# Performance work log

Hardware: AMD Instinct MI355X
Metric: run time of the kernel (lower is better)

## Reference

```python
import jax, jax.numpy as jnp
import numpy as np

MAX_STEPS = 20  # matches init kwarg max_steps


def gru_cell(x, h, W_ih, W_hh, b_ih, b_hh):
    # PyTorch GRUCell: gates ordered (reset, update, new)
    H = h.shape[1]
    gx = x @ W_ih.T + b_ih          # [B, 3H]
    gh = h @ W_hh.T + b_hh          # [B, 3H]
    r = jax.nn.sigmoid(gx[:, :H] + gh[:, :H])
    z = jax.nn.sigmoid(gx[:, H:2 * H] + gh[:, H:2 * H])
    n = jnp.tanh(gx[:, 2 * H:] + r * gh[:, 2 * H:])
    return (1.0 - z) * n + z * h


def setup_inputs() -> dict:
    key = jax.random.key(0)
    ks = jax.random.split(key, 10)
    B, E, H = 2048, 512, 1024
    bound = 1.0 / np.sqrt(H)  # torch default init scale
    uni = lambda k, shape: jax.random.uniform(k, shape, jnp.float32, -bound, bound)
    return {
        "x": jax.random.normal(ks[0], (B, E), jnp.float32),
        "W_ih": uni(ks[1], (3 * H, E)),
        "W_hh": uni(ks[2], (3 * H, H)),
        "b_ih": uni(ks[3], (3 * H,)),
        "b_hh": uni(ks[4], (3 * H,)),
        "w_out": uni(ks[5], (H,)),
        "b_out": uni(ks[6], (1,)),
        "w_lam": uni(ks[7], (H,)),
        "b_lam": uni(ks[8], (1,)),
        "u": jax.random.uniform(ks[9], (MAX_STEPS, B), jnp.float32),  # bernoulli draws
    }


def reference(x, W_ih, W_hh, b_ih, b_hh, w_out, b_out, w_lam, b_lam, u):
    B = x.shape[0]
    dt = x.dtype
    H = W_hh.shape[1]
    h0 = gru_cell(x, jnp.zeros((B, H), dt), W_ih, W_hh, b_ih, b_hh)
    steps = jnp.arange(1, MAX_STEPS + 1)

    def step(carry, inp):
        h, un_halted, halted, p_m, y_m = carry
        n_idx, u_n = inp
        lam_sig = jax.nn.sigmoid(h @ w_lam + b_lam[0])           # [B]
        lam = jnp.where(n_idx == MAX_STEPS, jnp.ones_like(lam_sig), lam_sig)
        y_n = h @ w_out + b_out[0]                                # [B]
        p_n = un_halted * lam
        un_halted = un_halted * (1.0 - lam)
        halt = (u_n < lam).astype(dt) * (1.0 - halted)            # bernoulli(lam)
        p_m = p_m * (1.0 - halt) + p_n * halt
        y_m = y_m * (1.0 - halt) + y_n * halt
        halted = halted + halt
        h = gru_cell(x, h, W_ih, W_hh, b_ih, b_hh)
        return (h, un_halted, halted, p_m, y_m), (p_n, y_n)

    init = (h0,
            jnp.ones((B,), dt),
            jnp.zeros((B,), dt),
            jnp.zeros((B,), dt),
            jnp.zeros((B,), dt))
    (_, _, _, p_m, y_m), (p, y) = jax.lax.scan(step, init, (steps, u))
    return p, y, p_m, y_m
```

## Files before the change

kernel.cpp:

```cpp
#include <hip/hip_runtime.h>
#include <math.h>


#define B_N 2048
#define E_N 512
#define H_N 1024
#define G3  3072
#define NSTEPS 20
#define BK 32
#define NT_H (H_N / BK)
#define NT_E (E_N / BK)
#define NCB  (H_N / 64)

typedef __attribute__((ext_vector_type(8))) _Float16 f16x8;
typedef __attribute__((ext_vector_type(4))) _Float16 f16x4v;
typedef __attribute__((ext_vector_type(4))) float    f32x4;

#define GLDS(src, dst) \
  __builtin_amdgcn_global_load_lds( \
      (const __attribute__((address_space(1))) void*)(src), \
      (__attribute__((address_space(3))) void*)(dst), 16, 0, 0)

__device__ __forceinline__ float sigmoidf_(float x) { return 1.0f / (1.0f + expf(-x)); }

__global__ __launch_bounds__(512, 2)
void gemm_step_mfma(const _Float16* __restrict__ h_hi_in,
                    const _Float16* __restrict__ h_lo_in,
                    const _Float16* __restrict__ Whi,
                    const _Float16* __restrict__ Wlo,
                    const float* __restrict__ b_hh,
                    const float* __restrict__ gx,
                    const float* __restrict__ w_lam,
                    const float* __restrict__ w_out,
                    _Float16* __restrict__ h_hi_out,
                    _Float16* __restrict__ h_lo_out,
                    float* __restrict__ part_lam,
                    float* __restrict__ part_out)
{
  __shared__ _Float16 lds[3][20480];
  __shared__ float pl_red[128][4], po_red[128][4];

  const int tid  = threadIdx.x;
  const int lane = tid & 63;
  const int wv   = tid >> 6;
  const int wr   = wv >> 2;
  const int wc   = wv & 3;
  const int row0 = blockIdx.y * 128;
  const int col0 = blockIdx.x * 64;
  const int cb   = blockIdx.x;

  const _Float16* srcp[5];
  int ldsoff[5];
  #pragma unroll
  for (int j = 0; j < 5; ++j) {
    const int c     = wv * 5 + j;
    const int row16 = lane >> 2;
    const int seg16 = lane & 3;
    const int seg   = (seg16 ^ (row16 & 3)) * 8;
    const _Float16* s;
    if (c < 8) {
      s = h_hi_in + (size_t)(row0 + c * 16 + row16) * H_N + seg;
    } else if (c < 16) {
      s = h_lo_in + (size_t)(row0 + (c - 8) * 16 + row16) * H_N + seg;
    } else if (c < 28) {
      const int br = (c - 16) * 16 + row16;
      s = Whi + (size_t)((br >> 6) * H_N + col0 + (br & 63)) * H_N + seg;
    } else {
      const int br = (c - 28) * 16 + row16;
      s = Wlo + (size_t)((br >> 6) * H_N + col0 + (br & 63)) * H_N + seg;
    }
    srcp[j]   = s;
    ldsoff[j] = c * 512;
  }

  f32x4 acc[3][4];
  #pragma unroll
  for (int g = 0; g < 3; ++g)
    #pragma unroll
    for (int mi = 0; mi < 4; ++mi)
      acc[g][mi] = (f32x4){0.f, 0.f, 0.f, 0.f};

  const int lrow = lane & 15;
  const int q    = lane >> 4;
  const int lkp  = (q ^ (lrow & 3)) * 8;
  const int capT = 2 * cb + (wc >> 1);
  float hold[4][4];

  auto issue = [&](int slot) {
    #pragma unroll
    for (int j = 0; j < 5; ++j) { GLDS(srcp[j], &lds[slot][ldsoff[j]]); srcp[j] += BK; }
  };

  auto body = [&](int t, bool do_issue) {
    __builtin_amdgcn_s_barrier();
    __builtin_amdgcn_sched_barrier(0);
    if (do_issue) issue((t + 2) % 3);
    const int sl = t % 3;
    f16x8 ah[4], al[4];
    #pragma unroll
    for (int mi = 0; mi < 4; ++mi) {
      const int r = wr * 64 + mi * 16 + lrow;
      ah[mi] = *(const f16x8*)&lds[sl][r * 32 + lkp];
      al[mi] = *(const f16x8*)&lds[sl][4096 + r * 32 + lkp];
    }
    f16x8 bh[3], bl[3];
    #pragma unroll
    for (int g = 0; g < 3; ++g) {
      const int br = g * 64 + wc * 16 + lrow;
      bh[g] = *(const f16x8*)&lds[sl][8192 + br * 32 + lkp];
      bl[g] = *(const f16x8*)&lds[sl][14336 + br * 32 + lkp];
    }
    if (t == capT) {
      #pragma unroll
      for (int mi = 0; mi < 4; ++mi)
        #pragma unroll
        for (int r = 0; r < 4; ++r) {
          const int arow = wr * 64 + mi * 16 + q * 4 + r;
          const int sslt = (((wc & 1) * 2 + (lrow >> 3)) ^ r) * 8 + (lrow & 7);
          hold[mi][r] = (float)lds[sl][arow * 32 + sslt]
                      + (float)lds[sl][4096 + arow * 32 + sslt];
        }
    }
    #pragma unroll
    for (int g = 0; g < 3; ++g)
      #pragma unroll
      for (int mi = 0; mi < 4; ++mi) {
        f32x4 c = acc[g][mi];
        c = __builtin_amdgcn_mfma_f32_16x16x32_f16(ah[mi], bh[g], c, 0, 0, 0);
        c = __builtin_amdgcn_mfma_f32_16x16x32_f16(ah[mi], bl[g], c, 0, 0, 0);
        c = __builtin_amdgcn_mfma_f32_16x16x32_f16(al[mi], bh[g], c, 0, 0, 0);
        acc[g][mi] = c;
      }
  };

  issue(0);
  issue(1);
  for (int t = 0; t < NT_H - 1; ++t) {
    asm volatile("s_waitcnt vmcnt(5)" ::: "memory");
    body(t, t < NT_H - 2);
  }
  asm volatile("s_waitcnt vmcnt(0)" ::: "memory");
  body(NT_H - 1, false);

  const int n   = col0 + wc * 16 + lrow;
  const float bhr = b_hh[n];
  const float bhz = b_hh[H_N + n];
  const float bhn = b_hh[2 * H_N + n];
  const float wl  = w_lam[n];
  const float wo  = w_out[n];
  #pragma unroll
  for (int mi = 0; mi < 4; ++mi) {
    #pragma unroll
    for (int r = 0; r < 4; ++r) {
      const int m = row0 + wr * 64 + mi * 16 + q * 4 + r;
      const float gr = acc[0][mi][r] + bhr;
      const float gz = acc[1][mi][r] + bhz;
      const float gn = acc[2][mi][r] + bhn;
      const size_t gxb = (size_t)m * G3;
      const float rr = sigmoidf_(gx[gxb + n] + gr);
      const float zz = sigmoidf_(gx[gxb + H_N + n] + gz);
      const float nn = tanhf(gx[gxb + 2 * H_N + n] + rr * gn);
      const float hf = (1.f - zz) * nn + zz * hold[mi][r];
      const _Float16 hh = (_Float16)hf;
      const size_t hidx = (size_t)m * H_N + n;
      h_hi_out[hidx] = hh;
      h_lo_out[hidx] = (_Float16)(hf - (float)hh);
      float pl = hf * wl;
      float po = hf * wo;
      #pragma unroll
      for (int mk = 1; mk < 16; mk <<= 1) {
        pl += __shfl_xor(pl, mk);
        po += __shfl_xor(po, mk);
      }
      if (lrow == 0) {
        pl_red[wr * 64 + mi * 16 + q * 4 + r][wc] = pl;
        po_red[wr * 64 + mi * 16 + q * 4 + r][wc] = po;
      }
    }
  }
  __syncthreads();
  if (tid < 128) {
    const int m = row0 + tid;
    part_lam[(size_t)cb * B_N + m] = (pl_red[tid][0] + pl_red[tid][1])
                                   + (pl_red[tid][2] + pl_red[tid][3]);
    part_out[(size_t)cb * B_N + m] = (po_red[tid][0] + po_red[tid][1])
                                   + (po_red[tid][2] + po_red[tid][3]);
  }
}

__global__ __launch_bounds__(256, 3)
void gemm_gx_mfma(const _Float16* __restrict__ xhi,
                  const _Float16* __restrict__ xlo,
                  const _Float16* __restrict__ Wihhi,
                  const _Float16* __restrict__ Wihlo,
                  const float* __restrict__ b_ih,
                  float* __restrict__ gx)
{
  __shared__ _Float16 lds[2][12288];

  const int tid  = threadIdx.x;
  const int lane = tid & 63;
  const int wv   = tid >> 6;
  const int wr   = wv >> 1;
  const int wc   = wv & 1;
  const int row0 = blockIdx.y * 128;
  const int col0 = blockIdx.x * 64;

  const _Float16* srcp[6];
  int ldsoff[6];
  #pragma unroll
  for (int j = 0; j < 6; ++j) {
    const int c     = wv * 6 + j;
    const int seg   = (lane & 3) * 8;
    const int row16 = lane >> 2;
    const _Float16* s;
    if (c < 8)       s = xhi   + (size_t)(row0 + c * 16 + row16) * E_N + seg;
    else if (c < 16) s = xlo   + (size_t)(row0 + (c - 8) * 16 + row16) * E_N + seg;
    else if (c < 20) s = Wihhi + (size_t)(col0 + (c - 16) * 16 + row16) * E_N + seg;
    else             s = Wihlo + (size_t)(col0 + (c - 20) * 16 + row16) * E_N + seg;
    srcp[j]   = s;
    ldsoff[j] = c * 512;
  }

  f32x4 acc[4][2];
  #pragma unroll
  for (int mi = 0; mi < 4; ++mi)
    #pragma unroll
    for (int ni = 0; ni < 2; ++ni) acc[mi][ni] = (f32x4){0.f, 0.f, 0.f, 0.f};

  const int lrow = lane & 15;
  const int lk   = (lane >> 4) * 8;
  const int q    = lane >> 4;

  #pragma unroll
  for (int j = 0; j < 6; ++j) { GLDS(srcp[j], &lds[0][ldsoff[j]]); srcp[j] += BK; }
  __syncthreads();

  for (int t = 0; t < NT_E; ++t) {
    const int p = t & 1;
    if (t + 1 < NT_E) {
      #pragma unroll
      for (int j = 0; j < 6; ++j) { GLDS(srcp[j], &lds[p ^ 1][ldsoff[j]]); srcp[j] += BK; }
    }
    f16x8 ah[4], al[4];
    #pragma unroll
    for (int mi = 0; mi < 4; ++mi) {
      const int r = wr * 64 + mi * 16 + lrow;
      ah[mi] = *(const f16x8*)&lds[p][r * 32 + lk];
      al[mi] = *(const f16x8*)&lds[p][4096 + r * 32 + lk];
    }
    f16x8 bh[2], bl[2];
    #pragma unroll
    for (int ni = 0; ni < 2; ++ni) {
      const int r = wc * 32 + ni * 16 + lrow;
      bh[ni] = *(const f16x8*)&lds[p][8192 + r * 32 + lk];
      bl[ni] = *(const f16x8*)&lds[p][10240 + r * 32 + lk];
    }
    #pragma unroll
    for (int mi = 0; mi < 4; ++mi)
      #pragma unroll
      for (int ni = 0; ni < 2; ++ni) {
        f32x4 c = acc[mi][ni];
        c = __builtin_amdgcn_mfma_f32_16x16x32_f16(ah[mi], bh[ni], c, 0, 0, 0);
        c = __builtin_amdgcn_mfma_f32_16x16x32_f16(ah[mi], bl[ni], c, 0, 0, 0);
        c = __builtin_amdgcn_mfma_f32_16x16x32_f16(al[mi], bh[ni], c, 0, 0, 0);
        acc[mi][ni] = c;
      }
    __syncthreads();
  }

  #pragma unroll
  for (int mi = 0; mi < 4; ++mi) {
    #pragma unroll
    for (int ni = 0; ni < 2; ++ni) {
      const int n = col0 + wc * 32 + ni * 16 + lrow;
      const float bi = b_ih[n];
      #pragma unroll
      for (int r = 0; r < 4; ++r) {
        const int m = row0 + wr * 64 + mi * 16 + q * 4 + r;
        gx[(size_t)m * G3 + n] = acc[mi][ni][r] + bi;
      }
    }
  }
}

__global__ __launch_bounds__(256)
void split_f32_kernel(const float* __restrict__ src,
                      _Float16* __restrict__ hi, _Float16* __restrict__ lo)
{
  const size_t base = ((size_t)blockIdx.x * 256 + threadIdx.x) * 4;
  const float4 w = *(const float4*)&src[base];
  float s[4] = {w.x, w.y, w.z, w.w};
  f16x4v h4, l4;
  #pragma unroll
  for (int e = 0; e < 4; ++e) {
    const _Float16 h = (_Float16)s[e];
    h4[e] = h;
    l4[e] = (_Float16)(s[e] - (float)h);
  }
  *(f16x4v*)&hi[base] = h4;
  *(f16x4v*)&lo[base] = l4;
}

__global__ __launch_bounds__(256)
void init_h0_kernel(const float* __restrict__ gx, const float* __restrict__ b_hh,
                    _Float16* __restrict__ h_hi, _Float16* __restrict__ h_lo,
                    float* __restrict__ states)
{
    const int idx = blockIdx.x * 256 + threadIdx.x;
    const int r = idx >> 10;
    const int c = idx & (H_N - 1);
    const float rr = sigmoidf_(gx[(size_t)r * G3 + c] + b_hh[c]);
    const float zz = sigmoidf_(gx[(size_t)r * G3 + H_N + c] + b_hh[H_N + c]);
    const float nn = tanhf(gx[(size_t)r * G3 + 2 * H_N + c] + rr * b_hh[2 * H_N + c]);
    const float hf = (1.0f - zz) * nn;
    const _Float16 hh = (_Float16)hf;
    h_hi[idx] = hh;
    h_lo[idx] = (_Float16)(hf - (float)hh);
    if (idx < B_N) {
        states[idx]           = 1.0f;
        states[B_N + idx]     = 0.0f;
        states[2 * B_N + idx] = 0.0f;
        states[3 * B_N + idx] = 0.0f;
    }
}

__global__ __launch_bounds__(256)
void halt_kernel(const int n,
                 const _Float16* __restrict__ h_hi, const _Float16* __restrict__ h_lo,
                 const float* __restrict__ w_out, const float* __restrict__ b_out,
                 const float* __restrict__ w_lam, const float* __restrict__ b_lam,
                 const float* __restrict__ u,
                 float* __restrict__ states,
                 float* __restrict__ out_p, float* __restrict__ out_y,
                 float* __restrict__ out_pm, float* __restrict__ out_ym)
{
    const int row = blockIdx.x;
    const int tid = threadIdx.x;
    const size_t base = (size_t)row * H_N + (tid << 2);
    const f16x4v hh4 = *(const f16x4v*)&h_hi[base];
    const f16x4v hl4 = *(const f16x4v*)&h_lo[base];
    const float4 wl = *(const float4*)&w_lam[tid << 2];
    const float4 wo = *(const float4*)&w_out[tid << 2];
    float hv[4];
    #pragma unroll
    for (int e = 0; e < 4; ++e) hv[e] = (float)hh4[e] + (float)hl4[e];
    float s_lam = hv[0] * wl.x + hv[1] * wl.y + hv[2] * wl.z + hv[3] * wl.w;
    float s_out = hv[0] * wo.x + hv[1] * wo.y + hv[2] * wo.z + hv[3] * wo.w;
    #pragma unroll
    for (int off = 32; off > 0; off >>= 1) {
        s_lam += __shfl_down(s_lam, off);
        s_out += __shfl_down(s_out, off);
    }
    __shared__ float redl[4], redo[4];
    const int wid = tid >> 6;
    if ((tid & 63) == 0) { redl[wid] = s_lam; redo[wid] = s_out; }
    __syncthreads();
    if (tid == 0) {
        const float dlam = redl[0] + redl[1] + redl[2] + redl[3];
        const float dout = redo[0] + redo[1] + redo[2] + redo[3];
        const float lam = (n == NSTEPS) ? 1.0f : sigmoidf_(dlam + b_lam[0]);
        const float y_n = dout + b_out[0];
        float un = states[row];
        float ha = states[B_N + row];
        float pm = states[2 * B_N + row];
        float ym = states[3 * B_N + row];
        const float p_n = un * lam;
        un = un * (1.0f - lam);
        const float halt = (u[(size_t)(n - 1) * B_N + row] < lam ? 1.0f : 0.0f) * (1.0f - ha);
        pm = pm * (1.0f - halt) + p_n * halt;
        ym = ym * (1.0f - halt) + y_n * halt;
        ha += halt;
        states[row] = un;
        states[B_N + row] = ha;
        states[2 * B_N + row] = pm;
        states[3 * B_N + row] = ym;
        out_p[(size_t)(n - 1) * B_N + row] = p_n;
        out_y[(size_t)(n - 1) * B_N + row] = y_n;
        if (n == NSTEPS) { out_pm[row] = pm; out_ym[row] = ym; }
    }
}

__global__ __launch_bounds__(256)
void finish_halt_kernel(const int n,
                        const float* __restrict__ part_lam,
                        const float* __restrict__ part_out,
                        const float* __restrict__ b_out, const float* __restrict__ b_lam,
                        const float* __restrict__ u,
                        float* __restrict__ states,
                        float* __restrict__ out_p, float* __restrict__ out_y,
                        float* __restrict__ out_pm, float* __restrict__ out_ym)
{
    const int row = blockIdx.x * 256 + threadIdx.x;
    float dlam = 0.f, dout = 0.f;
    #pragma unroll
    for (int cb = 0; cb < NCB; ++cb) {
        dlam += part_lam[(size_t)cb * B_N + row];
        dout += part_out[(size_t)cb * B_N + row];
    }
    const float lam = (n == NSTEPS) ? 1.0f : sigmoidf_(dlam + b_lam[0]);
    const float y_n = dout + b_out[0];
    float un = states[row];
    float ha = states[B_N + row];
    float pm = states[2 * B_N + row];
    float ym = states[3 * B_N + row];
    const float p_n = un * lam;
    un = un * (1.0f - lam);
    const float halt = (u[(size_t)(n - 1) * B_N + row] < lam ? 1.0f : 0.0f) * (1.0f - ha);
    pm = pm * (1.0f - halt) + p_n * halt;
    ym = ym * (1.0f - halt) + y_n * halt;
    ha += halt;
    states[row] = un;
    states[B_N + row] = ha;
    states[2 * B_N + row] = pm;
    states[3 * B_N + row] = ym;
    out_p[(size_t)(n - 1) * B_N + row] = p_n;
    out_y[(size_t)(n - 1) * B_N + row] = y_n;
    if (n == NSTEPS) { out_pm[row] = pm; out_ym[row] = ym; }
}

extern "C" void kernel_launch(void* const* d_in, const int* in_sizes, int n_in,
                              void* d_out, int out_size, void* d_ws, size_t ws_size,
                              hipStream_t stream) {
    const float* x     = (const float*)d_in[0];
    const float* W_ih  = (const float*)d_in[1];
    const float* W_hh  = (const float*)d_in[2];
    const float* b_ih  = (const float*)d_in[3];
    const float* b_hh  = (const float*)d_in[4];
    const float* w_out = (const float*)d_in[5];
    const float* b_out = (const float*)d_in[6];
    const float* w_lam = (const float*)d_in[7];
    const float* b_lam = (const float*)d_in[8];
    const float* u     = (const float*)d_in[9];

    float* out_p  = (float*)d_out;
    float* out_y  = out_p + (size_t)NSTEPS * B_N;
    float* out_pm = out_y + (size_t)NSTEPS * B_N;
    float* out_ym = out_pm + B_N;

    float* ws = (float*)d_ws;
    float*     gx   = ws;
    _Float16*  Whi  = (_Float16*)(gx + (size_t)B_N * G3);
    _Float16*  Wlo  = Whi + (size_t)G3 * H_N;
    _Float16*  hAhi = Wlo + (size_t)G3 * H_N;
    _Float16*  hAlo = hAhi + (size_t)B_N * H_N;
    _Float16*  hBhi = hAlo + (size_t)B_N * H_N;
    _Float16*  hBlo = hBhi + (size_t)B_N * H_N;
    float*     part_lam = (float*)(hBlo + (size_t)B_N * H_N);
    float*     part_out = part_lam + (size_t)NCB * B_N;
    float*     states   = part_out + (size_t)NCB * B_N;

    const dim3 blk(256);
    split_f32_kernel<<<dim3((size_t)G3 * H_N / 1024), blk, 0, stream>>>(W_hh, Whi, Wlo);
    split_f32_kernel<<<dim3((size_t)G3 * E_N / 1024), blk, 0, stream>>>(W_ih, hAhi, hAlo);
    split_f32_kernel<<<dim3((size_t)B_N * E_N / 1024), blk, 0, stream>>>(x, hBhi, hBlo);
    gemm_gx_mfma<<<dim3(G3 / 64, B_N / 128), blk, 0, stream>>>(hBhi, hBlo, hAhi, hAlo, b_ih, gx);
    init_h0_kernel<<<dim3(B_N * H_N / 256), blk, 0, stream>>>(gx, b_hh, hAhi, hAlo, states);

    _Float16 *hchi = hAhi, *hclo = hAlo, *hnhi = hBhi, *hnlo = hBlo;
    for (int n = 1; n <= NSTEPS; ++n) {
        if (n == 1) {
            halt_kernel<<<dim3(B_N), blk, 0, stream>>>(n, hchi, hclo, w_out, b_out,
                                                       w_lam, b_lam, u, states,
                                                       out_p, out_y, out_pm, out_ym);
        } else {
            finish_halt_kernel<<<dim3(B_N / 256), blk, 0, stream>>>(n, part_lam, part_out,
                                                                    b_out, b_lam, u, states,
                                                                    out_p, out_y, out_pm, out_ym);
        }
        if (n < NSTEPS) {
            gemm_step_mfma<<<dim3(H_N / 64, B_N / 128), dim3(512), 0, stream>>>(
                hchi, hclo, Whi, Wlo, b_hh, gx, w_lam, w_out, hnhi, hnlo, part_lam, part_out);
            _Float16* t;
            t = hchi; hchi = hnhi; hnhi = t;
            t = hclo; hclo = hnlo; hnlo = t;
        }
    }
}
```

Measured before the change: 1.280 ms.

## Store GEMM tiles in LDS in MFMA fragment order with double buffering

Tiles for h and W are now written to LDS in the order the MFMA fragments consume them, so each lane reads one contiguous 16-byte chunk instead of a swizzled row-major address. The three-stage ring with manual vmcnt waits becomes a two-buffer loop synchronised by __syncthreads, and launch bounds drop to one block per CU. The aim is to cut LDS bank conflicts and address arithmetic, and to give the kernel more registers. In exchange, prefetch depth is reduced and the full barrier drains every outstanding load each iteration, which can expose global-memory latency.

```diff
diff --git a/kernel.cpp b/kernel.cpp
--- a/kernel.cpp
+++ b/kernel.cpp
@@ -23,7 +23,7 @@
 
 __device__ __forceinline__ float sigmoidf_(float x) { return 1.0f / (1.0f + expf(-x)); }
 
-__global__ __launch_bounds__(512, 2)
+__global__ __launch_bounds__(512, 1)
 void gemm_step_mfma(const _Float16* __restrict__ h_hi_in,
                     const _Float16* __restrict__ h_lo_in,
                     const _Float16* __restrict__ Whi,
@@ -37,7 +37,7 @@
                     float* __restrict__ part_lam,
                     float* __restrict__ part_out)
 {
-  __shared__ _Float16 lds[3][20480];
+  __shared__ _Float16 lds[2][20480];
   __shared__ float pl_red[128][4], po_red[128][4];
 
   const int tid  = threadIdx.x;
@@ -49,25 +49,32 @@
   const int col0 = blockIdx.x * 64;
   const int cb   = blockIdx.x;
 
+  const int lrow = lane & 15;
+  const int q    = lane >> 4;
+
   const _Float16* srcp[5];
   int ldsoff[5];
   #pragma unroll
   for (int j = 0; j < 5; ++j) {
-    const int c     = wv * 5 + j;
-    const int row16 = lane >> 2;
-    const int seg16 = lane & 3;
-    const int seg   = (seg16 ^ (row16 & 3)) * 8;
+    const int c   = wv * 5 + j;
+    const int lrx = lane & 15;
+    const int qx  = lane >> 4;
     const _Float16* s;
     if (c < 8) {
-      s = h_hi_in + (size_t)(row0 + c * 16 + row16) * H_N + seg;
+      const int row = row0 + (c >> 2) * 64 + (c & 3) * 16 + lrx;
+      s = h_hi_in + (size_t)row * H_N + qx * 8;
     } else if (c < 16) {
-      s = h_lo_in + (size_t)(row0 + (c - 8) * 16 + row16) * H_N + seg;
+      const int cc = c - 8;
+      const int row = row0 + (cc >> 2) * 64 + (cc & 3) * 16 + lrx;
+      s = h_lo_in + (size_t)row * H_N + qx * 8;
     } else if (c < 28) {
-      const int br = (c - 16) * 16 + row16;
-      s = Whi + (size_t)((br >> 6) * H_N + col0 + (br & 63)) * H_N + seg;
+      const int cc = c - 16;
+      const int rowg = (cc >> 2) * H_N + col0 + (cc & 3) * 16 + lrx;
+      s = Whi + (size_t)rowg * H_N + qx * 8;
     } else {
-      const int br = (c - 28) * 16 + row16;
-      s = Wlo + (size_t)((br >> 6) * H_N + col0 + (br & 63)) * H_N + seg;
+      const int cc = c - 28;
+      const int rowg = (cc >> 2) * H_N + col0 + (cc & 3) * 16 + lrx;
+      s = Wlo + (size_t)rowg * H_N + qx * 8;
     }
     srcp[j]   = s;
     ldsoff[j] = c * 512;
@@ -80,47 +87,50 @@
     for (int mi = 0; mi < 4; ++mi)
       acc[g][mi] = (f32x4){0.f, 0.f, 0.f, 0.f};
 
-  const int lrow = lane & 15;
-  const int q    = lane >> 4;
-  const int lkp  = (q ^ (lrow & 3)) * 8;
   const int capT = 2 * cb + (wc >> 1);
   float hold[4][4];
 
-  auto issue = [&](int slot) {
-    #pragma unroll
-    for (int j = 0; j < 5; ++j) { GLDS(srcp[j], &lds[slot][ldsoff[j]]); srcp[j] += BK; }
+  auto issue = [&](int p) {
+    #pragma unroll
+    for (int j = 0; j < 5; ++j) { GLDS(srcp[j], &lds[p][ldsoff[j]]); srcp[j] += BK; }
   };
 
-  auto body = [&](int t, bool do_issue) {
-    __builtin_amdgcn_s_barrier();
-    __builtin_amdgcn_sched_barrier(0);
-    if (do_issue) issue((t + 2) % 3);
-    const int sl = t % 3;
+  issue(0);
+  __syncthreads();
+
+  for (int t = 0; t < NT_H; ++t) {
+    const int p = t & 1;
+    if (t + 1 < NT_H) issue(p ^ 1);
+
+    const _Float16* Lp = &lds[p][0];
+
     f16x8 ah[4], al[4];
     #pragma unroll
     for (int mi = 0; mi < 4; ++mi) {
-      const int r = wr * 64 + mi * 16 + lrow;
-      ah[mi] = *(const f16x8*)&lds[sl][r * 32 + lkp];
-      al[mi] = *(const f16x8*)&lds[sl][4096 + r * 32 + lkp];
+      const int u = ((wr * 4 + mi) * 64 + lane) * 8;
+      ah[mi] = *(const f16x8*)&Lp[u];
+      al[mi] = *(const f16x8*)&Lp[4096 + u];
     }
     f16x8 bh[3], bl[3];
     #pragma unroll
     for (int g = 0; g < 3; ++g) {
-      const int br = g * 64 + wc * 16 + lrow;
-      bh[g] = *(const f16x8*)&lds[sl][8192 + br * 32 + lkp];
-      bl[g] = *(const f16x8*)&lds[sl][14336 + br * 32 + lkp];
-    }
+      const int u = ((g * 4 + wc) * 64 + lane) * 8;
+      bh[g] = *(const f16x8*)&Lp[8192 + u];
+      bl[g] = *(const f16x8*)&Lp[14336 + u];
+    }
+
     if (t == capT) {
+      const int q2 = (wc & 1) * 2 + (lrow >> 3);
+      const int e  = lrow & 7;
       #pragma unroll
       for (int mi = 0; mi < 4; ++mi)
         #pragma unroll
         for (int r = 0; r < 4; ++r) {
-          const int arow = wr * 64 + mi * 16 + q * 4 + r;
-          const int sslt = (((wc & 1) * 2 + (lrow >> 3)) ^ r) * 8 + (lrow & 7);
-          hold[mi][r] = (float)lds[sl][arow * 32 + sslt]
-                      + (float)lds[sl][4096 + arow * 32 + sslt];
+          const int off = (((wr * 4 + mi) * 64) + q2 * 16 + q * 4 + r) * 8 + e;
+          hold[mi][r] = (float)Lp[off] + (float)Lp[4096 + off];
         }
     }
+
     #pragma unroll
     for (int g = 0; g < 3; ++g)
       #pragma unroll
@@ -131,16 +141,8 @@
         c = __builtin_amdgcn_mfma_f32_16x16x32_f16(al[mi], bh[g], c, 0, 0, 0);
         acc[g][mi] = c;
       }
-  };
-
-  issue(0);
-  issue(1);
-  for (int t = 0; t < NT_H - 1; ++t) {
-    asm volatile("s_waitcnt vmcnt(5)" ::: "memory");
-    body(t, t < NT_H - 2);
-  }
-  asm volatile("s_waitcnt vmcnt(0)" ::: "memory");
-  body(NT_H - 1, false);
+    __syncthreads();
+  }
 
   const int n   = col0 + wc * 16 + lrow;
   const float bhr = b_hh[n];
```

Measured after the change: 1.474 ms (median of 2 runs). 1.15x slower.
